# Kernel optimization log

Hardware: AMD Instinct MI355X
Metric: run time of the kernel (lower is better)

Reference implementation:

```python
import jax, jax.numpy as jnp
import numpy as np

EPS = 1e-5
K = 16
DILATION = 1

def _bn(x, g, b, axes):
    # BatchNorm in training mode: batch statistics over all axes except channel (last)
    m = jnp.mean(x, axis=axes, keepdims=True)
    v = jnp.var(x, axis=axes, keepdims=True)
    return (x - m) * jax.lax.rsqrt(v + EPS) * g + b

def _knn_idx(p, q, k):
    # p: [B,N,3], q: [B,M,3] -> indices [B,M,k] of nearest points in p for each q
    d = (jnp.sum(q * q, -1)[:, :, None]
         - 2.0 * jnp.einsum('bmc,bnc->bmn', q, p)
         + jnp.sum(p * p, -1)[:, None, :])  # [B,M,N]
    _, idx = jax.lax.top_k(-d, k)
    return jax.lax.stop_gradient(idx)

def setup_inputs() -> dict:
    key = jax.random.key(0)
    ks = jax.random.split(key, 16)
    B, N, M, Cin, Cout = 8, 8192, 2048, 64, 128
    mid, K2 = Cout // 4, K * K
    s = 0.02
    d = {
        'p': jax.random.normal(ks[0], (B, N, 3), jnp.float32),
        'q': jax.random.normal(ks[1], (B, M, 3), jnp.float32),
        'x': jax.random.normal(ks[2], (B, Cin, N), jnp.float32),
        # mlp: two 1x1 convs (3->mid->mid) each with BN
        'W1': jax.random.normal(ks[3], (mid, 3), jnp.float32) * s,
        'b1': jnp.zeros((mid,), jnp.float32),
        'g1': jnp.ones((mid,), jnp.float32), 'be1': jnp.zeros((mid,), jnp.float32),
        'W2': jax.random.normal(ks[4], (mid, mid), jnp.float32) * s,
        'b2': jnp.zeros((mid,), jnp.float32),
        'g2': jnp.ones((mid,), jnp.float32), 'be2': jnp.zeros((mid,), jnp.float32),
        # stn: conv [1,K] (3->K^2), then two 1x1 convs (K^2->K^2)
        'Ws1': jax.random.normal(ks[5], (K2, 3, K), jnp.float32) * s,
        'bs1': jnp.zeros((K2,), jnp.float32),
        'gs1': jnp.ones((K2,), jnp.float32), 'bes1': jnp.zeros((K2,), jnp.float32),
        'Ws2': jax.random.normal(ks[6], (K2, K2), jnp.float32) * s,
        'bs2': jnp.zeros((K2,), jnp.float32),
        'gs2': jnp.ones((K2,), jnp.float32), 'bes2': jnp.zeros((K2,), jnp.float32),
        'Ws3': jax.random.normal(ks[7], (K2, K2), jnp.float32) * s,
        'bs3': jnp.zeros((K2,), jnp.float32),
        # final conv [1,K]: (Cin+mid -> Cout) with BN
        'Wc': jax.random.normal(ks[8], (Cout, Cin + mid, K), jnp.float32) * s,
        'bc': jnp.zeros((Cout,), jnp.float32),
        'gc': jnp.ones((Cout,), jnp.float32), 'bec': jnp.zeros((Cout,), jnp.float32),
    }
    return d

def reference(p, q, x, W1, b1, g1, be1, W2, b2, g2, be2,
              Ws1, bs1, gs1, bes1, Ws2, bs2, gs2, bes2, Ws3, bs3,
              Wc, bc, gc, bec):
    B, M = q.shape[0], q.shape[1]
    idx = _knn_idx(p, q, K * DILATION)[..., ::DILATION]  # [B,M,K]
    # gather neighbor coords and center: p_hat [B,M,K,3]
    p_n = jax.vmap(lambda a, i: a[i])(p, idx)
    p_hat = p_n - q[:, :, None, :]
    # mlp (pointwise convs, channel-last)
    h = jax.nn.relu(_bn(jnp.einsum('bmkc,oc->bmko', p_hat, W1) + b1, g1, be1, (0, 1, 2)))
    h = jax.nn.relu(_bn(jnp.einsum('bmkc,oc->bmko', h, W2) + b2, g2, be2, (0, 1, 2)))
    # gather features: x [B,Cin,N] -> [B,M,K,Cin]
    xt = jnp.transpose(x, (0, 2, 1))
    x_n = jax.vmap(lambda a, i: a[i])(xt, idx)
    x_hat = jnp.concatenate([h, x_n], axis=-1)  # [B,M,K,mid+Cin]
    # stn -> transform T [B,M,K,K]
    t = jax.nn.relu(_bn(jnp.einsum('bmkc,ock->bmo', p_hat, Ws1) + bs1, gs1, bes1, (0, 1)))
    t = jax.nn.relu(_bn(jnp.einsum('bmi,oi->bmo', t, Ws2) + bs2, gs2, bes2, (0, 1)))
    t = jnp.einsum('bmi,oi->bmo', t, Ws3) + bs3  # [B,M,K*K]
    T = t.reshape(B, M, K, K)
    x2 = jnp.einsum('bmij,bmjc->bmic', T, x_hat)  # [B,M,K,mid+Cin]
    out = jax.nn.relu(_bn(jnp.einsum('bmkc,ock->bmo', x2, Wc) + bc, gc, bec, (0, 1)))  # [B,M,Cout]
    return (q, jnp.transpose(out, (0, 2, 1)))  # q, x:[B,Cout,M]
```

## Files before the change

kernel.cpp:

```cpp
#include <hip/hip_runtime.h>
#include <hip/hip_bf16.h>


#define EPS 1e-5f

constexpr int Bb   = 8;
constexpr int Np   = 8192;
constexpr int Mq   = 2048;
constexpr int COUT = 128;
constexpr int BM   = Bb * Mq;
constexpr int BMK  = BM * 16;
constexpr int GC   = 16;
constexpr int NC   = GC * GC * GC;
constexpr int CAP  = 320;

typedef __attribute__((ext_vector_type(8))) short short8;
typedef __attribute__((ext_vector_type(4))) float f32x4;

__device__ __forceinline__ unsigned short f2bf(float x) {
  unsigned u = __float_as_uint(x);
  u += 0x7fffu + ((u >> 16) & 1u);
  return (unsigned short)(u >> 16);
}
__device__ __forceinline__ float bf2f_lo(unsigned v) { return __uint_as_float(v << 16); }
__device__ __forceinline__ float bf2f_hi(unsigned v) { return __uint_as_float(v & 0xffff0000u); }

__device__ __forceinline__ int cell_of(float c) {
  int v = (int)floorf(c * 2.0f + 8.0f);
  return v < 0 ? 0 : (v > 15 ? 15 : v);
}

__device__ __forceinline__ unsigned enc_dist(float d) {
  unsigned uu = __float_as_uint(d);
  return uu ^ (((unsigned)(((int)uu) >> 31)) | 0x80000000u);
}

__device__ __forceinline__ void bsort64(unsigned long long& v, int lane) {
#pragma unroll
  for (int k = 2; k <= 64; k <<= 1) {
#pragma unroll
    for (int jj = k >> 1; jj > 0; jj >>= 1) {
      unsigned long long o = __shfl_xor(v, jj);
      bool keepMin = (((lane & k) == 0) == ((lane & jj) == 0));
      unsigned long long mn = v < o ? v : o;
      unsigned long long mx = v < o ? o : v;
      v = keepMin ? mn : mx;
    }
  }
}
__device__ __forceinline__ void bmerge64(unsigned long long& v, int lane) {
#pragma unroll
  for (int jj = 32; jj > 0; jj >>= 1) {
    unsigned long long o = __shfl_xor(v, jj);
    bool keepMin = ((lane & jj) == 0);
    unsigned long long mn = v < o ? v : o;
    unsigned long long mx = v < o ? o : v;
    v = keepMin ? mn : mx;
  }
}
__device__ __forceinline__ unsigned long long sort_smallest64(const unsigned long long* buf,
                                                              int C, int lane) {
  unsigned long long run = (lane < C) ? buf[lane] : ~0ULL;
  bsort64(run, lane);
  for (int b2 = 64; b2 < C; b2 += 64) {
    unsigned long long v = (b2 + lane < C) ? buf[b2 + lane] : ~0ULL;
    bsort64(v, lane);
    unsigned long long vr = __shfl_xor(v, 63);
    unsigned long long m = run < vr ? run : vr;
    bmerge64(m, lane);
    run = m;
  }
  return run;
}


__device__ __forceinline__ void bn1_compute(int o, const float* __restrict__ st,
                                            const float* __restrict__ W1,
                                            const float* __restrict__ b1,
                                            const float* __restrict__ g1,
                                            const float* __restrict__ be1,
                                            float* sc_out, float* shf_out) {
  float n = (float)BMK;
  float w0 = W1[3 * o], w1 = W1[3 * o + 1], w2 = W1[3 * o + 2], b = b1[o];
  float s0 = st[0], s1 = st[1], s2 = st[2];
  float m00 = st[3], m11 = st[4], m22 = st[5], m01 = st[6], m02 = st[7], m12 = st[8];
  float ws = (w0 * s0 + w1 * s1 + w2 * s2) / n;
  float mean = b + ws;
  float quad = w0 * w0 * m00 + w1 * w1 * m11 + w2 * w2 * m22 +
               2.f * (w0 * w1 * m01 + w0 * w2 * m02 + w1 * w2 * m12);
  float ex2 = quad / n + 2.f * b * ws + b * b;
  float var = ex2 - mean * mean;
  float sc = g1[o] * rsqrtf(var + EPS);
  *sc_out = sc;
  *shf_out = be1[o] - mean * sc + b * sc;
}

__global__ __launch_bounds__(256) void prep_kernel(const float* __restrict__ p,
                                                   const float* __restrict__ x,
                                                   const float* __restrict__ Wc,
                                                   float4* __restrict__ pp4,
                                                   float* __restrict__ xt,
                                                   unsigned short* __restrict__ wcrp,
                                                   int* __restrict__ hist) {
  __shared__ float tile[64][65];
  int blk = blockIdx.x;
  int tid = threadIdx.x;
  if (blk < 256) {
    int i = blk * 256 + tid;
    float px = p[3 * i], py = p[3 * i + 1], pz = p[3 * i + 2];
    float pp = __fadd_rn(__fadd_rn(__fmul_rn(px, px), __fmul_rn(py, py)), __fmul_rn(pz, pz));
    pp4[i] = make_float4(px, py, pz, pp);
    int b = i >> 13;
    int cid = (cell_of(px) << 8) | (cell_of(py) << 4) | cell_of(pz);
    atomicAdd(&hist[b * NC + cid], 1);
  } else if (blk < 1280) {
    int bx = blk - 256;
    int b = bx >> 7;
    int n0 = (bx & 127) << 6;
    int nl = tid & 63;
    int r0 = tid >> 6;
    const float* xb = x + (size_t)b * 64 * Np;
    for (int c = r0; c < 64; c += 4) tile[c][nl] = xb[(size_t)c * Np + n0 + nl];
    __syncthreads();
    float* xtb = xt + (size_t)b * Np * 64;
    for (int n = r0; n < 64; n += 4) xtb[(size_t)(n0 + n) * 64 + nl] = tile[nl][n];
  } else {
    int g = (blk - 1280) * 256 + tid;
    if (g < 128 * 1536) {
      int o = g / 1536, r = g % 1536;
      int c = r % 96, j = r / 96;
      wcrp[g] = f2bf(Wc[(size_t)o * 1536 + c * 16 + j]);
    }
  }
}

__global__ __launch_bounds__(256) void prefix_kernel(const int* __restrict__ hist,
                                                     int* __restrict__ cellstart,
                                                     int* __restrict__ cursor) {
  __shared__ int ls[256];
  int b = blockIdx.x, t = threadIdx.x;
  const int* h = hist + b * NC;
  int loc[16], s = 0;
#pragma unroll
  for (int k = 0; k < 16; ++k) { loc[k] = h[t * 16 + k]; s += loc[k]; }
  ls[t] = s;
  __syncthreads();
  for (int off = 1; off < 256; off <<= 1) {
    int v = (t >= off) ? ls[t - off] : 0;
    __syncthreads();
    ls[t] += v;
    __syncthreads();
  }
  int run = ls[t] - s;
  int* cs = cellstart + b * (NC + 1);
  int* cu = cursor + b * NC;
#pragma unroll
  for (int k = 0; k < 16; ++k) {
    cs[t * 16 + k] = run;
    cu[t * 16 + k] = run;
    run += loc[k];
  }
  if (t == 255) cs[NC] = run;
}

__global__ __launch_bounds__(256) void scatter_kernel(const float4* __restrict__ pp4,
                                                      int* __restrict__ cursor,
                                                      float4* __restrict__ sp4,
                                                      int* __restrict__ sidx) {
  int i = blockIdx.x * 256 + threadIdx.x;
  int b = i >> 13;
  float4 pv = pp4[i];
  int cid = (cell_of(pv.x) << 8) | (cell_of(pv.y) << 4) | cell_of(pv.z);
  int pos = atomicAdd(&cursor[b * NC + cid], 1);
  sp4[(size_t)b * Np + pos] = pv;
  sidx[(size_t)b * Np + pos] = i & 8191;
}

__global__ __launch_bounds__(256) void knn_kernel(const float4* __restrict__ pp4,
                                                  const float4* __restrict__ sp4,
                                                  const int* __restrict__ cellstart,
                                                  const float* __restrict__ q,
                                                  int* __restrict__ idx_out) {
  __shared__ unsigned long long cand[8][CAP];
  int tid = threadIdx.x;
  int wslot = tid >> 6;
  int wave = blockIdx.x * 4 + wslot;
  int lane = tid & 63;
  int q0 = wave * 2;
  int b = q0 >> 11;
  const float4* pb = pp4 + (size_t)b * Np;
  const float4* sp = sp4 + (size_t)b * Np;
  const int* cs = cellstart + b * (NC + 1);
  float qx[2], qy[2], qz[2], qqv[2];
#pragma unroll
  for (int j = 0; j < 2; ++j) {
    const float* qp = q + (size_t)(q0 + j) * 3;
    qx[j] = qp[0]; qy[j] = qp[1]; qz[j] = qp[2];
    qqv[j] = __fadd_rn(__fadd_rn(__fmul_rn(qx[j], qx[j]), __fmul_rn(qy[j], qy[j])),
                       __fmul_rn(qz[j], qz[j]));
  }
  float tau_f[2] = {INFINITY, INFINITY};

  for (int j = 0; j < 2; ++j) {
    int cx = cell_of(qx[j]), cy = cell_of(qy[j]), cz = cell_of(qz[j]);
    int alo = 0, blo = 0, nbw = 1, ncols = 1, zlo = 0, zhi = 0;
    int myS = 0, myE = 0;
    for (int r = 0;; ++r) {
      alo = cx - r; if (alo < 0) alo = 0;
      int ahi = cx + r; if (ahi > 15) ahi = 15;
      blo = cy - r; if (blo < 0) blo = 0;
      int bhi = cy + r; if (bhi > 15) bhi = 15;
      zlo = cz - r; if (zlo < 0) zlo = 0;
      zhi = cz + r; if (zhi > 15) zhi = 15;
      nbw = bhi - blo + 1;
      ncols = (ahi - alo + 1) * nbw;
      int total = 0;
      for (int l0 = 0; l0 < ncols; l0 += 64) {
        int l = l0 + lane;
        int sL = 0, eL = 0;
        if (l < ncols) {
          int da = l / nbw, db = l - da * nbw;
          int cbase = ((alo + da) << 8) | ((blo + db) << 4);
          sL = cs[cbase + zlo];
          eL = cs[cbase + zhi + 1];
        }
        if (l0 == 0) { myS = sL; myE = eL; }
        total += eL - sL;
      }
#pragma unroll
      for (int o = 32; o > 0; o >>= 1) total += __shfl_xor(total, o);
      if (total >= 16 || r >= 15) break;
    }
    unsigned u0 = 0xFFFFFFFFu, u1 = 0xFFFFFFFFu;
    int wcnt = 0;
    int ccen = (cx - alo) * nbw + (cy - blo);
    for (int c2 = 0; c2 < ncols && wcnt < 128; ++c2) {
      int cc = (c2 == 0) ? ccen : (c2 <= ccen ? c2 - 1 : c2);
      int s0, e;
      if (cc < 64) {
        s0 = __shfl(myS, cc);
        e = __shfl(myE, cc);
      } else {
        int da = cc / nbw, db = cc - da * nbw;
        int cbase = ((alo + da) << 8) | ((blo + db) << 4);
        s0 = cs[cbase + zlo];
        e = cs[cbase + zhi + 1];
      }
      for (int off = s0; off < e && wcnt < 128; off += 64) {
        int rem = e - off; if (rem > 64) rem = 64;
        int rot = wcnt & 63;
        int rel = (lane - rot) & 63;
        int g = wcnt + rel;
        if (rel < rem && g < 128) {
          float4 pv = sp[off + rel];
          float ee = __fmaf_rn(qz[j], pv.z, __fmaf_rn(qy[j], pv.y, __fmul_rn(qx[j], pv.x)));
          float d = __fadd_rn(__fsub_rn(qqv[j], __fmul_rn(2.0f, ee)), pv.w);
          unsigned uu = enc_dist(d);
          if (g < 64) u0 = uu; else u1 = uu;
        }
        wcnt += rem;
      }
    }
    unsigned lo = 0u, hi = 0xFF800000u;
    for (int it = 0; it < 20; ++it) {
      unsigned mid = lo + ((hi - lo) >> 1);
      int c = (int)__popcll(__ballot(u0 <= mid)) + (int)__popcll(__ballot(u1 <= mid));
      if (c >= 16) hi = mid; else lo = mid + 1;
    }
    tau_f[j] = (hi >= 0x80000000u) ? __uint_as_float(hi ^ 0x80000000u)
                                   : __uint_as_float(~hi);
  }

  int cnt[2] = {0, 0};
  unsigned long long lanebelow = (1ULL << lane) - 1ULL;
  for (int base = 0; base < Np; base += 256) {
    float4 pv[4];
#pragma unroll
    for (int u4 = 0; u4 < 4; ++u4) pv[u4] = pb[base + u4 * 64 + lane];
    float d[4][2];
#pragma unroll
    for (int u4 = 0; u4 < 4; ++u4)
#pragma unroll
      for (int j = 0; j < 2; ++j) {
        float e = __fmaf_rn(qz[j], pv[u4].z, __fmaf_rn(qy[j], pv[u4].y, __fmul_rn(qx[j], pv[u4].x)));
        d[u4][j] = __fadd_rn(__fsub_rn(qqv[j], __fmul_rn(2.0f, e)), pv[u4].w);
      }
#pragma unroll
    for (int u4 = 0; u4 < 4; ++u4)
#pragma unroll
      for (int j = 0; j < 2; ++j) {
        unsigned long long mask = __ballot(d[u4][j] <= tau_f[j]);
        if (mask) {
          if (d[u4][j] <= tau_f[j]) {
            int i = base + u4 * 64 + lane;
            unsigned uu = enc_dist(d[u4][j]);
            int wp = cnt[j] + (int)__popcll(mask & lanebelow);
            if (wp < CAP)
              cand[wslot * 2 + j][wp] = (((unsigned long long)uu) << 32) | (unsigned)i;
          }
          cnt[j] += (int)__popcll(mask);
        }
      }
  }
  __syncthreads();

  for (int j = 0; j < 2; ++j) {
    int slot = wslot * 2 + j;
    if (cnt[j] <= CAP) {
      unsigned long long run = sort_smallest64(&cand[slot][0], cnt[j], lane);
      if (lane < 16)
        idx_out[(size_t)(q0 + j) * 16 + lane] = (int)(run & 0xffffffffULL);
    } else {
      unsigned long long kk = ~0ULL;
      float tl = tau_f[j];
      for (int base = 0; base < Np; base += 64) {
        float4 pv = pb[base + lane];
        float ee = __fmaf_rn(qz[j], pv.z, __fmaf_rn(qy[j], pv.y, __fmul_rn(qx[j], pv.x)));
        float dv = __fadd_rn(__fsub_rn(qqv[j], __fmul_rn(2.0f, ee)), pv.w);
        unsigned long long mask = __ballot(dv <= tl);
        if (mask) {
          unsigned uu = enc_dist(dv);
          unsigned long long cd = (((unsigned long long)uu) << 32) | (unsigned)(base + lane);
          do {
            int src = __ffsll((unsigned long long)mask) - 1;
            mask &= mask - 1;
            unsigned long long ck = __shfl(cd, src);
            unsigned long long up = __shfl_up(kk, 1);
            if (lane == 0) up = 0ULL;
            if (lane < 16 && ck < kk) kk = (up > ck) ? up : ck;
          } while (mask);
          unsigned long long tt = __shfl(kk, 15);
          unsigned tm = (unsigned)(tt >> 32);
          unsigned inv2 = tm ^ ((tm & 0x80000000u) ? 0x80000000u : 0xFFFFFFFFu);
          float tc = (tm == 0xFFFFFFFFu) ? INFINITY : __uint_as_float(inv2);
          if (tc < tl) tl = tc;
        }
      }
      if (lane < 16)
        idx_out[(size_t)(q0 + j) * 16 + lane] = (int)(kk & 0xffffffffULL);
    }
  }
}

__global__ __launch_bounds__(256) void phat_stats_kernel(const float4* __restrict__ pp4,
                                                         const float* __restrict__ q,
                                                         const int* __restrict__ idx,
                                                         float* __restrict__ phat,
                                                         float* __restrict__ stats) {
  float a[9];
#pragma unroll
  for (int k = 0; k < 9; ++k) a[k] = 0.f;
  int tid = threadIdx.x;
  for (int it = 0; it < 4; ++it) {
    int bmk = blockIdx.x * 256 + tid + it * 65536;
    int bm = bmk >> 4;
    int b = bm >> 11;
    int j = idx[bmk];
    float4 pv = pp4[(size_t)b * Np + j];
    const float* qp = q + (size_t)bm * 3;
    float h0 = pv.x - qp[0], h1 = pv.y - qp[1], h2 = pv.z - qp[2];
    phat[(size_t)bmk * 3 + 0] = h0;
    phat[(size_t)bmk * 3 + 1] = h1;
    phat[(size_t)bmk * 3 + 2] = h2;
    a[0] += h0; a[1] += h1; a[2] += h2;
    a[3] += h0 * h0; a[4] += h1 * h1; a[5] += h2 * h2;
    a[6] += h0 * h1; a[7] += h0 * h2; a[8] += h1 * h2;
  }
#pragma unroll
  for (int off = 32; off > 0; off >>= 1)
#pragma unroll
    for (int k = 0; k < 9; ++k) a[k] += __shfl_down(a[k], off);
  __shared__ float ls[9];
  if (tid < 9) ls[tid] = 0.f;
  __syncthreads();
  if ((tid & 63) == 0)
    for (int k = 0; k < 9; ++k) atomicAdd(&ls[k], a[k]);
  __syncthreads();
  if (tid < 9) atomicAdd(&stats[tid], ls[tid]);
}

__global__ __launch_bounds__(256) void stats2_kernel(const float* __restrict__ phat,
                                                     const float* __restrict__ stats,
                                                     const float* __restrict__ W1,
                                                     const float* __restrict__ b1,
                                                     const float* __restrict__ g1,
                                                     const float* __restrict__ be1,
                                                     const float* __restrict__ W2,
                                                     const float* __restrict__ b2,
                                                     float* __restrict__ stats2) {
  __shared__ float hsh[256 * 36];
  __shared__ float w2s[32 * 33];
  __shared__ float w1s[96], sc1[32], sh1[32], b2s[32], ls[64];
  int tid = threadIdx.x;
  if (tid < 32) {
    bn1_compute(tid, stats, W1, b1, g1, be1, &sc1[tid], &sh1[tid]);
    b2s[tid] = b2[tid];
  }
  if (tid < 96) w1s[tid] = W1[tid];
  if (tid < 64) ls[tid] = 0.f;
  for (int e = tid; e < 1024; e += 256) w2s[(e >> 5) * 33 + (e & 31)] = W2[e];
  __syncthreads();
  {
    int bmk = blockIdx.x * 256 + tid;
    float h0 = phat[(size_t)bmk * 3], hy = phat[(size_t)bmk * 3 + 1], hz = phat[(size_t)bmk * 3 + 2];
#pragma unroll
    for (int o4 = 0; o4 < 8; ++o4) {
      float4 r;
      float* rp = (float*)&r;
#pragma unroll
      for (int u = 0; u < 4; ++u) {
        int o = o4 * 4 + u;
        float t = w1s[3 * o] * h0 + w1s[3 * o + 1] * hy + w1s[3 * o + 2] * hz;
        rp[u] = fmaxf(0.f, t * sc1[o] + sh1[o]);
      }
      *(float4*)&hsh[tid * 36 + o4 * 4] = r;
    }
  }
  __syncthreads();
  int oc = tid & 31, grp = tid >> 5;
  float wrow[32];
#pragma unroll
  for (int c = 0; c < 32; ++c) wrow[c] = w2s[oc * 33 + c];
  float bias = b2s[oc];
  float ss = 0.f, qq = 0.f;
  for (int r = 0; r < 32; ++r) {
    int row = grp * 32 + r;
    float a = bias;
    const float4* hr = (const float4*)&hsh[row * 36];
#pragma unroll
    for (int c4 = 0; c4 < 8; ++c4) {
      float4 hv = hr[c4];
      a += hv.x * wrow[c4 * 4 + 0];
      a += hv.y * wrow[c4 * 4 + 1];
      a += hv.z * wrow[c4 * 4 + 2];
      a += hv.w * wrow[c4 * 4 + 3];
    }
    ss += a;
    qq += a * a;
  }
  atomicAdd(&ls[oc], ss);
  atomicAdd(&ls[32 + oc], qq);
  __syncthreads();
  if (tid < 64) atomicAdd(&stats2[tid], ls[tid]);
}

__global__ __launch_bounds__(256) void stn1_kernel(const float* __restrict__ phat,
                                                   const float* __restrict__ Ws1,
                                                   const float* __restrict__ bs1,
                                                   float* __restrict__ pt1,
                                                   float* __restrict__ spt1) {
  __shared__ float w[256 * 49];
  __shared__ float ph[32 * 48];
  int tid = threadIdx.x;
  int bm0 = blockIdx.x * 32;
  for (int e = tid; e < 256 * 48; e += 256) w[(e / 48) * 49 + (e % 48)] = Ws1[e];
  for (int e = tid; e < 32 * 48; e += 256) ph[e] = phat[(size_t)bm0 * 48 + e];
  __syncthreads();
  int o = tid;
  float acc[32];
  float bias = bs1[o];
#pragma unroll
  for (int j = 0; j < 32; ++j) acc[j] = bias;
#pragma unroll
  for (int c = 0; c < 3; ++c)
#pragma unroll
    for (int k = 0; k < 16; ++k) {
      float wv = w[o * 49 + c * 16 + k];
#pragma unroll
      for (int j = 0; j < 32; ++j) acc[j] += ph[j * 48 + k * 3 + c] * wv;
    }
  float s = 0.f, s2 = 0.f;
  for (int j = 0; j < 32; ++j) {
    pt1[(size_t)(bm0 + j) * 256 + o] = acc[j];
    s += acc[j];
    s2 += acc[j] * acc[j];
  }
  atomicAdd(&spt1[o], s);
  atomicAdd(&spt1[256 + o], s2);
}

__global__ __launch_bounds__(256) void stn_mm_kernel(const float* __restrict__ in,
                                                     const float* __restrict__ sums,
                                                     const float* __restrict__ gg,
                                                     const float* __restrict__ be,
                                                     const float* __restrict__ W,
                                                     const float* __restrict__ bias,
                                                     float* __restrict__ out,
                                                     float* __restrict__ outstats,
                                                     int do_stats) {
  __shared__ unsigned short As[64 * 40], Bs[128 * 40];
  __shared__ float scA[256], shA[256], ls[256];
  int tid = threadIdx.x;
  ls[tid] = 0.f;
  {
    float n = (float)BM;
    float mean = sums[tid] / n;
    float var = sums[256 + tid] / n - mean * mean;
    float s = gg[tid] * rsqrtf(var + EPS);
    scA[tid] = s;
    shA[tid] = be[tid] - mean * s;
  }
  int mb = blockIdx.x >> 1, nb = blockIdx.x & 1;
  int bm0 = mb * 64, o0 = nb * 128;
  int wid = tid >> 6, lane = tid & 63;
  int wm = wid >> 1, wn = wid & 1;
  int mh = lane & 15, quad = lane >> 4;
  f32x4 acc[2][4];
#pragma unroll
  for (int a = 0; a < 2; ++a)
#pragma unroll
    for (int bq = 0; bq < 4; ++bq) acc[a][bq] = (f32x4){0.f, 0.f, 0.f, 0.f};
  int ar = tid >> 2, aseg = tid & 3;
  const float* Ag = in + (size_t)(bm0 + ar) * 256 + aseg * 8;
  int aoff = ar * 40 + aseg * 8;
  int ci = aseg * 8;
  for (int i0 = 0; i0 < 256; i0 += 32) {
    __syncthreads();
    float4 v0 = *(const float4*)(Ag + i0);
    float4 v1 = *(const float4*)(Ag + i0 + 4);
    float av[8] = {v0.x, v0.y, v0.z, v0.w, v1.x, v1.y, v1.z, v1.w};
    short8 ap;
#pragma unroll
    for (int k = 0; k < 8; ++k)
      ap[k] = (short)f2bf(fmaxf(0.f, av[k] * scA[i0 + ci + k] + shA[i0 + ci + k]));
    *(short8*)&As[aoff] = ap;
#pragma unroll
    for (int jb = 0; jb < 2; ++jb) {
      int br = jb * 64 + ar;
      const float* Bg = W + (size_t)(o0 + br) * 256 + aseg * 8;
      float4 u0 = *(const float4*)(Bg + i0);
      float4 u1 = *(const float4*)(Bg + i0 + 4);
      float bv[8] = {u0.x, u0.y, u0.z, u0.w, u1.x, u1.y, u1.z, u1.w};
      short8 bp;
#pragma unroll
      for (int k = 0; k < 8; ++k) bp[k] = (short)f2bf(bv[k]);
      *(short8*)&Bs[br * 40 + aseg * 8] = bp;
    }
    __syncthreads();
#pragma unroll
    for (int mt = 0; mt < 2; ++mt) {
      short8 af = *(const short8*)&As[(wm * 32 + mt * 16 + mh) * 40 + quad * 8];
#pragma unroll
      for (int nt = 0; nt < 4; ++nt) {
        short8 bf = *(const short8*)&Bs[(wn * 64 + nt * 16 + mh) * 40 + quad * 8];
        acc[mt][nt] = __builtin_amdgcn_mfma_f32_16x16x32_bf16(af, bf, acc[mt][nt], 0, 0, 0);
      }
    }
  }
#pragma unroll
  for (int mt = 0; mt < 2; ++mt)
#pragma unroll
    for (int nt = 0; nt < 4; ++nt) {
      int colL = wn * 64 + nt * 16 + mh;
      int col = o0 + colL;
      float bvv = bias[col];
      float ps = 0.f, pq = 0.f;
#pragma unroll
      for (int r = 0; r < 4; ++r) {
        float val = acc[mt][nt][r] + bvv;
        out[(size_t)(bm0 + wm * 32 + mt * 16 + quad * 4 + r) * 256 + col] = val;
        ps += val;
        pq += val * val;
      }
      if (do_stats) {
        atomicAdd(&ls[colL], ps);
        atomicAdd(&ls[128 + colL], pq);
      }
    }
  if (do_stats) {
    __syncthreads();
    if (tid < 128) {
      atomicAdd(&outstats[o0 + tid], ls[tid]);
      atomicAdd(&outstats[256 + o0 + tid], ls[128 + tid]);
    }
  }
}

__global__ __launch_bounds__(256) void xhat_x2_kernel(const float* __restrict__ phat,
                                                      const float* __restrict__ stats,
                                                      const float* __restrict__ stats2,
                                                      const float* __restrict__ W1,
                                                      const float* __restrict__ b1,
                                                      const float* __restrict__ g1,
                                                      const float* __restrict__ be1,
                                                      const float* __restrict__ W2,
                                                      const float* __restrict__ b2,
                                                      const float* __restrict__ g2,
                                                      const float* __restrict__ be2,
                                                      const float* __restrict__ xt,
                                                      const int* __restrict__ idx,
                                                      const float* __restrict__ Tbuf,
                                                      unsigned short* __restrict__ x2) {
  __shared__ unsigned short xh[256 * 98];
  __shared__ float w1s[96], w2s[32 * 33], sc1[32], sh1[32], sc2[32], sh2[32];
  int tid = threadIdx.x;
  if (tid < 32) {
    bn1_compute(tid, stats, W1, b1, g1, be1, &sc1[tid], &sh1[tid]);
    float n = (float)BMK;
    float mean = stats2[tid] / n;
    float var = stats2[32 + tid] / n - mean * mean;
    float s = g2[tid] * rsqrtf(var + EPS);
    sc2[tid] = s;
    sh2[tid] = be2[tid] - mean * s + b2[tid] * s;
  }
  if (tid < 96) w1s[tid] = W1[tid];
  for (int e = tid; e < 1024; e += 256) w2s[(e >> 5) * 33 + (e & 31)] = W2[e];
  __syncthreads();
  int bm0 = blockIdx.x * 16;
  int b = bm0 >> 11;
  int bml = tid >> 4, j = tid & 15;
  int bmk = (bm0 + bml) * 16 + j;
  int row = tid * 98;
  {
    float h0 = phat[(size_t)bmk * 3], hy = phat[(size_t)bmk * 3 + 1], hz = phat[(size_t)bmk * 3 + 2];
    float h1[32];
#pragma unroll
    for (int o = 0; o < 32; ++o) {
      float t = w1s[3 * o] * h0 + w1s[3 * o + 1] * hy + w1s[3 * o + 2] * hz;
      h1[o] = fmaxf(0.f, t * sc1[o] + sh1[o]);
    }
#pragma unroll
    for (int o4 = 0; o4 < 8; ++o4) {
      float r[4];
#pragma unroll
      for (int u = 0; u < 4; ++u) {
        int o = o4 * 4 + u;
        float a = 0.f;
#pragma unroll
        for (int c = 0; c < 32; ++c) a += h1[c] * w2s[o * 33 + c];
        r[u] = fmaxf(0.f, a * sc2[o] + sh2[o]);
      }
      *(unsigned*)&xh[row + o4 * 4] = (unsigned)f2bf(r[0]) | (((unsigned)f2bf(r[1])) << 16);
      *(unsigned*)&xh[row + o4 * 4 + 2] = (unsigned)f2bf(r[2]) | (((unsigned)f2bf(r[3])) << 16);
    }
    int jx = idx[bmk];
    const float4* xr = (const float4*)(xt + ((size_t)b * Np + jx) * 64);
#pragma unroll
    for (int c4 = 0; c4 < 16; ++c4) {
      float4 v = xr[c4];
      *(unsigned*)&xh[row + 32 + c4 * 4] = (unsigned)f2bf(v.x) | (((unsigned)f2bf(v.y)) << 16);
      *(unsigned*)&xh[row + 32 + c4 * 4 + 2] = (unsigned)f2bf(v.z) | (((unsigned)f2bf(v.w)) << 16);
    }
  }
  float Tr[16];
  {
    const float4* tg = (const float4*)(Tbuf + (size_t)(bm0 + bml) * 256 + j * 16);
#pragma unroll
    for (int w4 = 0; w4 < 4; ++w4) {
      float4 tv = tg[w4];
      Tr[w4 * 4 + 0] = tv.x; Tr[w4 * 4 + 1] = tv.y;
      Tr[w4 * 4 + 2] = tv.z; Tr[w4 * 4 + 3] = tv.w;
    }
  }
  __syncthreads();
#pragma unroll
  for (int c0 = 0; c0 < 96; c0 += 32) {
    float acc[32];
#pragma unroll
    for (int cc = 0; cc < 32; ++cc) acc[cc] = 0.f;
#pragma unroll
    for (int jj = 0; jj < 16; ++jj) {
      const unsigned* xr2 = (const unsigned*)&xh[(bml * 16 + jj) * 98 + c0];
      float t = Tr[jj];
#pragma unroll
      for (int cc = 0; cc < 16; ++cc) {
        unsigned uv = xr2[cc];
        acc[cc * 2] += t * bf2f_lo(uv);
        acc[cc * 2 + 1] += t * bf2f_hi(uv);
      }
    }
    unsigned* dst = (unsigned*)(x2 + (size_t)bmk * 96 + c0);
#pragma unroll
    for (int cc = 0; cc < 16; ++cc)
      dst[cc] = (unsigned)f2bf(acc[cc * 2]) | (((unsigned)f2bf(acc[cc * 2 + 1])) << 16);
  }
}

__global__ __launch_bounds__(256) void preout_kernel(const unsigned short* __restrict__ x2,
                                                     const unsigned short* __restrict__ Wcrp,
                                                     const float* __restrict__ bc,
                                                     float* __restrict__ pout,
                                                     float* __restrict__ spout) {
  __shared__ unsigned short As[64 * 40], Bs[128 * 40];
  __shared__ float ls[256];
  int tid = threadIdx.x;
  ls[tid] = 0.f;
  int bm0 = blockIdx.x * 64;
  int wid = tid >> 6, lane = tid & 63;
  int wm = wid >> 1, wn = wid & 1;
  int mh = lane & 15, quad = lane >> 4;
  f32x4 acc[2][4];
#pragma unroll
  for (int a = 0; a < 2; ++a)
#pragma unroll
    for (int bq = 0; bq < 4; ++bq) acc[a][bq] = (f32x4){0.f, 0.f, 0.f, 0.f};
  int ar = tid >> 2, aseg = tid & 3;
  const unsigned short* Ag = x2 + (size_t)(bm0 + ar) * 1536 + aseg * 8;
  const unsigned short* Bg0 = Wcrp + (size_t)ar * 1536 + aseg * 8;
  const unsigned short* Bg1 = Wcrp + (size_t)(64 + ar) * 1536 + aseg * 8;
  int aoff = ar * 40 + aseg * 8;
  short8 a_pre = *(const short8*)Ag;
  short8 b_pre0 = *(const short8*)Bg0;
  short8 b_pre1 = *(const short8*)Bg1;
  for (int i0 = 0; i0 < 1536; i0 += 32) {
    __syncthreads();
    *(short8*)&As[aoff] = a_pre;
    *(short8*)&Bs[aoff] = b_pre0;
    *(short8*)&Bs[64 * 40 + aoff] = b_pre1;
    __syncthreads();
    if (i0 + 32 < 1536) {
      a_pre = *(const short8*)(Ag + i0 + 32);
      b_pre0 = *(const short8*)(Bg0 + i0 + 32);
      b_pre1 = *(const short8*)(Bg1 + i0 + 32);
    }
#pragma unroll
    for (int mt = 0; mt < 2; ++mt) {
      short8 af = *(const short8*)&As[(wm * 32 + mt * 16 + mh) * 40 + quad * 8];
#pragma unroll
      for (int nt = 0; nt < 4; ++nt) {
        short8 bf = *(const short8*)&Bs[(wn * 64 + nt * 16 + mh) * 40 + quad * 8];
        acc[mt][nt] = __builtin_amdgcn_mfma_f32_16x16x32_bf16(af, bf, acc[mt][nt], 0, 0, 0);
      }
    }
  }
#pragma unroll
  for (int mt = 0; mt < 2; ++mt)
#pragma unroll
    for (int nt = 0; nt < 4; ++nt) {
      int col = wn * 64 + nt * 16 + mh;
      float bvv = bc[col];
      float ps = 0.f, pq = 0.f;
#pragma unroll
      for (int r = 0; r < 4; ++r) {
        float val = acc[mt][nt][r] + bvv;
        pout[(size_t)(bm0 + wm * 32 + mt * 16 + quad * 4 + r) * 128 + col] = val;
        ps += val;
        pq += val * val;
      }
      atomicAdd(&ls[col], ps);
      atomicAdd(&ls[128 + col], pq);
    }
  __syncthreads();
  atomicAdd(&spout[tid], ls[tid]);
}

__global__ __launch_bounds__(256) void final_kernel(const float* __restrict__ q,
                                                    const float* __restrict__ pout,
                                                    const float* __restrict__ scs,
                                                    const float* __restrict__ gc,
                                                    const float* __restrict__ bec,
                                                    float* __restrict__ dout) {
  __shared__ float ldsT[128 * 65];
  int blk = blockIdx.x;
  int tid = threadIdx.x;
  if (blk < 192) {
    int g = blk * 256 + tid;
    dout[g] = q[g];
    return;
  }
  int blk2 = blk - 192;
  int b = blk2 >> 5;
  int m0 = (blk2 & 31) * 64;
  int row = tid >> 2, seg = tid & 3;
  const float4* src = (const float4*)(pout + ((size_t)(b * Mq) + m0 + row) * 128 + seg * 32);
#pragma unroll
  for (int k4 = 0; k4 < 8; ++k4) {
    float4 v = src[k4];
    int o = seg * 32 + k4 * 4;
    ldsT[(o + 0) * 65 + row] = v.x;
    ldsT[(o + 1) * 65 + row] = v.y;
    ldsT[(o + 2) * 65 + row] = v.z;
    ldsT[(o + 3) * 65 + row] = v.w;
  }
  __syncthreads();
  int lane = tid & 63, wv = tid >> 6;
  float n = (float)BM;
  float* base = dout + (size_t)BM * 3 + (size_t)b * COUT * Mq + m0;
#pragma unroll
  for (int rep = 0; rep < 32; ++rep) {
    int o = wv * 32 + rep;
    float mean = scs[o] / n;
    float var = scs[128 + o] / n - mean * mean;
    float s = gc[o] * rsqrtf(var + EPS);
    float shv = bec[o] - mean * s;
    float v = ldsT[o * 65 + lane];
    base[(size_t)o * Mq + lane] = fmaxf(0.f, v * s + shv);
  }
}

extern "C" void kernel_launch(void* const* d_in, const int* in_sizes, int n_in, void* d_out,
                              int out_size, void* d_ws, size_t ws_size, hipStream_t stream) {
  const float* p = (const float*)d_in[0];
  const float* q = (const float*)d_in[1];
  const float* x = (const float*)d_in[2];
  const float* W1 = (const float*)d_in[3];
  const float* b1 = (const float*)d_in[4];
  const float* g1 = (const float*)d_in[5];
  const float* be1 = (const float*)d_in[6];
  const float* W2 = (const float*)d_in[7];
  const float* b2 = (const float*)d_in[8];
  const float* g2 = (const float*)d_in[9];
  const float* be2 = (const float*)d_in[10];
  const float* Ws1 = (const float*)d_in[11];
  const float* bs1 = (const float*)d_in[12];
  const float* gs1 = (const float*)d_in[13];
  const float* bes1 = (const float*)d_in[14];
  const float* Ws2 = (const float*)d_in[15];
  const float* bs2 = (const float*)d_in[16];
  const float* gs2 = (const float*)d_in[17];
  const float* bes2 = (const float*)d_in[18];
  const float* Ws3 = (const float*)d_in[19];
  const float* bs3 = (const float*)d_in[20];
  const float* Wc = (const float*)d_in[21];
  const float* bc = (const float*)d_in[22];
  const float* gc = (const float*)d_in[23];
  const float* bec = (const float*)d_in[24];
  float* dout = (float*)d_out;

  char* ws = (char*)d_ws;
  float* stats = (float*)ws;
  size_t off = 8192;
  float4* pp4 = (float4*)(ws + off);  off += (size_t)Bb * Np * 16;
  int* idxb = (int*)(ws + off);       off += (size_t)BMK * 4;
  float* xt = (float*)(ws + off);     off += (size_t)Bb * Np * 64 * 4;
  float* phat = (float*)(ws + off);   off += (size_t)BMK * 3 * 4;
  float* pt1 = (float*)(ws + off);    off += (size_t)BM * 256 * 4;
  float* pt2 = (float*)(ws + off);    off += (size_t)BM * 256 * 4;
  float* Tb = (float*)(ws + off);     off += (size_t)BM * 256 * 4;
  float* pout = (float*)(ws + off);   off += (size_t)BM * 128 * 4;
  unsigned short* wcrp = (unsigned short*)(ws + off); off += (size_t)1536 * 128 * 2;
  unsigned short* x2 = (unsigned short*)(ws + off);   off += (size_t)BM * 1536 * 2;
  int* hist = (int*)(ws + off);       off += (size_t)Bb * NC * 4;
  int* cursor = (int*)(ws + off);     off += (size_t)Bb * NC * 4;
  int* cellstart = (int*)(ws + off);  off += (size_t)Bb * (NC + 1) * 4;
  float4* sp4 = (float4*)(ws + off);  off += (size_t)Bb * Np * 16;
  int* sidx = (int*)(ws + off);       off += (size_t)Bb * Np * 4;

  hipMemsetAsync(stats, 0, 8192, stream);
  hipMemsetAsync(hist, 0, (size_t)Bb * NC * 4, stream);
  hipLaunchKernelGGL(prep_kernel, dim3(2048), dim3(256), 0, stream, p, x, Wc, pp4, xt, wcrp, hist);
  hipLaunchKernelGGL(prefix_kernel, dim3(8), dim3(256), 0, stream, hist, cellstart, cursor);
  hipLaunchKernelGGL(scatter_kernel, dim3(256), dim3(256), 0, stream, pp4, cursor, sp4, sidx);
  hipLaunchKernelGGL(knn_kernel, dim3(2048), dim3(256), 0, stream, pp4, sp4, cellstart, q, idxb);
  hipLaunchKernelGGL(phat_stats_kernel, dim3(256), dim3(256), 0, stream, pp4, q, idxb, phat, stats);
  hipLaunchKernelGGL(stn1_kernel, dim3(512), dim3(256), 0, stream, phat, Ws1, bs1, pt1, stats + 128);
  hipLaunchKernelGGL(stats2_kernel, dim3(1024), dim3(256), 0, stream, phat, stats, W1, b1, g1, be1, W2, b2, stats + 16);
  hipLaunchKernelGGL(stn_mm_kernel, dim3(512), dim3(256), 0, stream, pt1, stats + 128, gs1, bes1, Ws2, bs2, pt2, stats + 640, 1);
  hipLaunchKernelGGL(stn_mm_kernel, dim3(512), dim3(256), 0, stream, pt2, stats + 640, gs2, bes2, Ws3, bs3, Tb, (float*)nullptr, 0);
  hipLaunchKernelGGL(xhat_x2_kernel, dim3(1024), dim3(256), 0, stream, phat, stats, stats + 16,
                     W1, b1, g1, be1, W2, b2, g2, be2, xt, idxb, Tb, x2);
  hipLaunchKernelGGL(preout_kernel, dim3(256), dim3(256), 0, stream, x2, wcrp, bc, pout, stats + 1152);
  hipLaunchKernelGGL(final_kernel, dim3(448), dim3(256), 0, stream, q, pout, stats + 1152, gc, bec, dout);
}
```

Before: 440.4 us.

## Run STN first conv on bf16 MFMA with split hi/lo precision

Replaces the scalar FP32 FMA loop in stn1_kernel with bf16 MFMA 16x16x32 instructions. Both phat and Ws1 are split into bf16 high and low parts, and three MFMAs per tile recover near-FP32 accuracy. Ws1 is pre-split and reordered into a padded 64-wide K layout inside prep_kernel. Each block now handles a 64x128 output tile instead of 32 rows by 256 outputs. This cuts ALU cost and the large per-block LDS weight load, at the price of extra conversion work and K padding from 48 to 64.

```diff
diff --git a/kernel.cpp b/kernel.cpp
--- a/kernel.cpp
+++ b/kernel.cpp
@@ -98,9 +98,11 @@
 __global__ __launch_bounds__(256) void prep_kernel(const float* __restrict__ p,
                                                    const float* __restrict__ x,
                                                    const float* __restrict__ Wc,
+                                                   const float* __restrict__ Ws1,
                                                    float4* __restrict__ pp4,
                                                    float* __restrict__ xt,
                                                    unsigned short* __restrict__ wcrp,
+                                                   unsigned short* __restrict__ ws1r,
                                                    int* __restrict__ hist) {
   __shared__ float tile[64][65];
   int blk = blockIdx.x;
@@ -124,13 +126,26 @@
     __syncthreads();
     float* xtb = xt + (size_t)b * Np * 64;
     for (int n = r0; n < 64; n += 4) xtb[(size_t)(n0 + n) * 64 + nl] = tile[nl][n];
-  } else {
+  } else if (blk < 2048) {
     int g = (blk - 1280) * 256 + tid;
     if (g < 128 * 1536) {
       int o = g / 1536, r = g % 1536;
       int c = r % 96, j = r / 96;
       wcrp[g] = f2bf(Wc[(size_t)o * 1536 + c * 16 + j]);
     }
+  } else {
+    int g = (blk - 2048) * 256 + tid;
+    int o = g >> 6, i = g & 63;
+    float val = 0.f;
+    if (i < 48) {
+      int k = i / 3, c = i - 3 * k;
+      val = Ws1[(size_t)o * 48 + c * 16 + k];
+    }
+    unsigned short h = f2bf(val);
+    float hf = __uint_as_float(((unsigned)h) << 16);
+    unsigned short l = f2bf(val - hf);
+    ws1r[g] = h;
+    ws1r[16384 + g] = l;
   }
 }
 
@@ -445,38 +460,102 @@
 }
 
 __global__ __launch_bounds__(256) void stn1_kernel(const float* __restrict__ phat,
-                                                   const float* __restrict__ Ws1,
+                                                   const unsigned short* __restrict__ ws1r,
                                                    const float* __restrict__ bs1,
                                                    float* __restrict__ pt1,
                                                    float* __restrict__ spt1) {
-  __shared__ float w[256 * 49];
-  __shared__ float ph[32 * 48];
+  __shared__ unsigned short Ah[64 * 72], Al[64 * 72], Bh[128 * 72], Bl[128 * 72];
+  __shared__ float ls[256];
   int tid = threadIdx.x;
-  int bm0 = blockIdx.x * 32;
-  for (int e = tid; e < 256 * 48; e += 256) w[(e / 48) * 49 + (e % 48)] = Ws1[e];
-  for (int e = tid; e < 32 * 48; e += 256) ph[e] = phat[(size_t)bm0 * 48 + e];
-  __syncthreads();
-  int o = tid;
-  float acc[32];
-  float bias = bs1[o];
-#pragma unroll
-  for (int j = 0; j < 32; ++j) acc[j] = bias;
-#pragma unroll
-  for (int c = 0; c < 3; ++c)
-#pragma unroll
-    for (int k = 0; k < 16; ++k) {
-      float wv = w[o * 49 + c * 16 + k];
-#pragma unroll
-      for (int j = 0; j < 32; ++j) acc[j] += ph[j * 48 + k * 3 + c] * wv;
-    }
-  float s = 0.f, s2 = 0.f;
-  for (int j = 0; j < 32; ++j) {
-    pt1[(size_t)(bm0 + j) * 256 + o] = acc[j];
-    s += acc[j];
-    s2 += acc[j] * acc[j];
-  }
-  atomicAdd(&spt1[o], s);
-  atomicAdd(&spt1[256 + o], s2);
+  ls[tid] = 0.f;
+  int mb = blockIdx.x >> 1, nb = blockIdx.x & 1;
+  int bm0 = mb * 64, o0 = nb * 128;
+  {
+    int zr = tid >> 2, zc = 48 + (tid & 3) * 4;
+    *(unsigned long long*)&Ah[zr * 72 + zc] = 0ULL;
+    *(unsigned long long*)&Al[zr * 72 + zc] = 0ULL;
+  }
+  {
+    int ar = tid >> 2, aseg = tid & 3;
+    const float* Ap = phat + (size_t)(bm0 + ar) * 48 + aseg * 12;
+    float4 v0 = *(const float4*)(Ap);
+    float4 v1 = *(const float4*)(Ap + 4);
+    float4 v2 = *(const float4*)(Ap + 8);
+    float av[12] = {v0.x, v0.y, v0.z, v0.w, v1.x, v1.y, v1.z, v1.w, v2.x, v2.y, v2.z, v2.w};
+    unsigned long long ph[3] = {0ULL, 0ULL, 0ULL}, pl[3] = {0ULL, 0ULL, 0ULL};
+#pragma unroll
+    for (int t = 0; t < 12; ++t) {
+      unsigned short h = f2bf(av[t]);
+      float hf = __uint_as_float(((unsigned)h) << 16);
+      unsigned short l = f2bf(av[t] - hf);
+      ph[t >> 2] |= ((unsigned long long)h) << ((t & 3) * 16);
+      pl[t >> 2] |= ((unsigned long long)l) << ((t & 3) * 16);
+    }
+    int base = ar * 72 + aseg * 12;
+#pragma unroll
+    for (int t4 = 0; t4 < 3; ++t4) {
+      *(unsigned long long*)&Ah[base + t4 * 4] = ph[t4];
+      *(unsigned long long*)&Al[base + t4 * 4] = pl[t4];
+    }
+  }
+#pragma unroll
+  for (int pass = 0; pass < 4; ++pass) {
+    int g = pass * 2048 + tid * 8;
+    int br = g >> 6, i2 = g & 63;
+    short8 vh = *(const short8*)&ws1r[(size_t)(o0 + br) * 64 + i2];
+    short8 vl = *(const short8*)&ws1r[16384 + (size_t)(o0 + br) * 64 + i2];
+    *(short8*)&Bh[br * 72 + i2] = vh;
+    *(short8*)&Bl[br * 72 + i2] = vl;
+  }
+  __syncthreads();
+  int wid = tid >> 6, lane = tid & 63;
+  int wm = wid >> 1, wn = wid & 1;
+  int mh = lane & 15, quad = lane >> 4;
+  f32x4 acc[2][4];
+#pragma unroll
+  for (int a = 0; a < 2; ++a)
+#pragma unroll
+    for (int bq = 0; bq < 4; ++bq) acc[a][bq] = (f32x4){0.f, 0.f, 0.f, 0.f};
+#pragma unroll
+  for (int kc = 0; kc < 2; ++kc) {
+    int ko = kc * 32 + quad * 8;
+#pragma unroll
+    for (int mt = 0; mt < 2; ++mt) {
+      short8 ah = *(const short8*)&Ah[(wm * 32 + mt * 16 + mh) * 72 + ko];
+      short8 al = *(const short8*)&Al[(wm * 32 + mt * 16 + mh) * 72 + ko];
+#pragma unroll
+      for (int nt = 0; nt < 4; ++nt) {
+        short8 bh = *(const short8*)&Bh[(wn * 64 + nt * 16 + mh) * 72 + ko];
+        short8 bl = *(const short8*)&Bl[(wn * 64 + nt * 16 + mh) * 72 + ko];
+        acc[mt][nt] = __builtin_amdgcn_mfma_f32_16x16x32_bf16(ah, bh, acc[mt][nt], 0, 0, 0);
+        acc[mt][nt] = __builtin_amdgcn_mfma_f32_16x16x32_bf16(ah, bl, acc[mt][nt], 0, 0, 0);
+        acc[mt][nt] = __builtin_amdgcn_mfma_f32_16x16x32_bf16(al, bh, acc[mt][nt], 0, 0, 0);
+      }
+    }
+  }
+#pragma unroll
+  for (int mt = 0; mt < 2; ++mt)
+#pragma unroll
+    for (int nt = 0; nt < 4; ++nt) {
+      int colL = wn * 64 + nt * 16 + mh;
+      int col = o0 + colL;
+      float bvv = bs1[col];
+      float ps = 0.f, pq = 0.f;
+#pragma unroll
+      for (int r = 0; r < 4; ++r) {
+        float val = acc[mt][nt][r] + bvv;
+        pt1[(size_t)(bm0 + wm * 32 + mt * 16 + quad * 4 + r) * 256 + col] = val;
+        ps += val;
+        pq += val * val;
+      }
+      atomicAdd(&ls[colL], ps);
+      atomicAdd(&ls[128 + colL], pq);
+    }
+  __syncthreads();
+  if (tid < 128) {
+    atomicAdd(&spt1[o0 + tid], ls[tid]);
+    atomicAdd(&spt1[256 + o0 + tid], ls[128 + tid]);
+  }
 }
 
 __global__ __launch_bounds__(256) void stn_mm_kernel(const float* __restrict__ in,
@@ -835,15 +914,16 @@
   int* cellstart = (int*)(ws + off);  off += (size_t)Bb * (NC + 1) * 4;
   float4* sp4 = (float4*)(ws + off);  off += (size_t)Bb * Np * 16;
   int* sidx = (int*)(ws + off);       off += (size_t)Bb * Np * 4;
+  unsigned short* ws1r = (unsigned short*)(ws + off); off += (size_t)2 * 256 * 64 * 2;
 
   hipMemsetAsync(stats, 0, 8192, stream);
   hipMemsetAsync(hist, 0, (size_t)Bb * NC * 4, stream);
-  hipLaunchKernelGGL(prep_kernel, dim3(2048), dim3(256), 0, stream, p, x, Wc, pp4, xt, wcrp, hist);
+  hipLaunchKernelGGL(prep_kernel, dim3(2112), dim3(256), 0, stream, p, x, Wc, Ws1, pp4, xt, wcrp, ws1r, hist);
   hipLaunchKernelGGL(prefix_kernel, dim3(8), dim3(256), 0, stream, hist, cellstart, cursor);
   hipLaunchKernelGGL(scatter_kernel, dim3(256), dim3(256), 0, stream, pp4, cursor, sp4, sidx);
   hipLaunchKernelGGL(knn_kernel, dim3(2048), dim3(256), 0, stream, pp4, sp4, cellstart, q, idxb);
   hipLaunchKernelGGL(phat_stats_kernel, dim3(256), dim3(256), 0, stream, pp4, q, idxb, phat, stats);
-  hipLaunchKernelGGL(stn1_kernel, dim3(512), dim3(256), 0, stream, phat, Ws1, bs1, pt1, stats + 128);
+  hipLaunchKernelGGL(stn1_kernel, dim3(512), dim3(256), 0, stream, phat, ws1r, bs1, pt1, stats + 128);
   hipLaunchKernelGGL(stats2_kernel, dim3(1024), dim3(256), 0, stream, phat, stats, W1, b1, g1, be1, W2, b2, stats + 16);
   hipLaunchKernelGGL(stn_mm_kernel, dim3(512), dim3(256), 0, stream, pt1, stats + 128, gs1, bes1, Ws2, bs2, pt2, stats + 640, 1);
   hipLaunchKernelGGL(stn_mm_kernel, dim3(512), dim3(256), 0, stream, pt2, stats + 640, gs2, bes2, Ws3, bs3, Tb, (float*)nullptr, 0);
```

Measured after the change: 381.1 us. -13.5%, faster.
